# Kernel optimization log

Measured on AMD Instinct MI355X. Metric: run time of the kernel, lower is better.

The kernel has to match this reference:

```python
import jax, jax.numpy as jnp
import numpy as np

B, L, D = 8, 1024, 512
H, DK, DV = 8, 64, 64
EPS = 1e-6
NEG = -1e9


def setup_inputs() -> dict:
    key = jax.random.key(0)
    ks = jax.random.split(key, 12)
    def xavier(k, shape):
        fan_out, fan_in = shape
        bound = float(np.sqrt(6.0 / (fan_in + fan_out)))
        return jax.random.uniform(k, shape, jnp.float32, -bound, bound)
    return {
        "q": jax.random.normal(ks[0], (B, L, D), jnp.float32),
        "k": jax.random.normal(ks[1], (B, L, D), jnp.float32),
        "v": jax.random.normal(ks[2], (B, L, D), jnp.float32),
        "event_type": jax.random.randint(ks[3], (B, L), 0, 2, jnp.int32),
        "mask": jax.random.randint(ks[4], (B, L, L), 0, 2, jnp.int32).astype(bool),
        "w_qs": xavier(ks[5], (H * DK, D)),
        "w_ex_en_qs": xavier(ks[6], (H * DK, D)),
        "w_ks": xavier(ks[7], (H * DK, D)),
        "w_vs": xavier(ks[8], (H * DV, D)),
        "w_fc": xavier(ks[9], (D, H * DV)),
        "b_fc": jnp.zeros((D,), jnp.float32),
        "ln_gamma": jnp.ones((D,), jnp.float32),
        "ln_beta": jnp.zeros((D,), jnp.float32),
    }


def _layer_norm(x, gamma, beta):
    mu = jnp.mean(x, axis=-1, keepdims=True)
    var = jnp.var(x, axis=-1, keepdims=True)
    return (x - mu) * jax.lax.rsqrt(var + EPS) * gamma + beta


def reference(q, k, v, event_type, mask, w_qs, w_ex_en_qs, w_ks, w_vs, w_fc, b_fc, ln_gamma, ln_beta):
    residual = q
    qn = _layer_norm(q, ln_gamma, ln_beta)  # normalize_before=True

    # event-type flags: en_en = prev is en AND present is en; ex_en = prev is ex AND present is en
    is_en = event_type != 0                                   # [B, L]
    en_en = (is_en[:, :, None] & is_en[:, None, :])[:, None]  # [B, 1, L, L]
    ex_en = ((~is_en)[:, :, None] & is_en[:, None, :])[:, None]

    def proj(x, w, d):  # torch Linear: x @ w.T, then split heads -> [B, H, L, d]
        return (x @ w.T).reshape(B, L, H, d).transpose(0, 2, 1, 3)

    q_en = proj(qn, w_qs, DK)
    q_ex = proj(qn, w_ex_en_qs, DK)
    kh = proj(k, w_ks, DK)
    vh = proj(v, w_vs, DV)

    temp = jnp.asarray(DK ** 0.5, qn.dtype)
    scores_en = jnp.einsum('bhqd,bhkd->bhqk', q_en / temp, kh)
    scores_en = jnp.where(mask[:, None], NEG, scores_en)      # masked branch
    scores_ex = jnp.einsum('bhqd,bhkd->bhqk', q_ex / temp, kh)  # unmasked branch

    blended = en_en * scores_en + ex_en * scores_ex           # [B, H, L, L]
    attn = jax.nn.softmax(blended, axis=-1)

    out = jnp.einsum('bhqk,bhkd->bhqd', attn, vh)             # PV
    out = out.transpose(0, 2, 1, 3).reshape(B, L, H * DV)
    out = out @ w_fc.T + b_fc
    out = out + residual
    return out, attn
```

## Files before the change

### kernel.cpp

```cpp
#include <hip/hip_runtime.h>

typedef __attribute__((ext_vector_type(8))) short bf16x8;
typedef __attribute__((ext_vector_type(4))) float f32x4;

#define DEVI static __device__ __forceinline__

constexpr float NEGV = -1e9f;

DEVI unsigned short f2b(float f) {
  union { float f; unsigned int u; } c; c.f = f;
  unsigned int lsb = (c.u >> 16) & 1u;
  return (unsigned short)((c.u + 0x7fffu + lsb) >> 16);
}
DEVI float sb2f(short s) {
  union { unsigned int u; float f; } c;
  c.u = ((unsigned int)(unsigned short)s) << 16;
  return c.f;
}

DEVI void gload16(const unsigned short* g, unsigned short* l) {
  __builtin_amdgcn_global_load_lds(
      (const __attribute__((address_space(1))) unsigned int*)g,
      (__attribute__((address_space(3))) unsigned int*)l, 16, 0, 0);
}

#define KSYNC(N) asm volatile("s_waitcnt vmcnt(" #N ") lgkmcnt(0)\n\ts_barrier" ::: "memory")

__global__ void mask_detect(const unsigned int* __restrict__ m, int n, int* flag) {
  unsigned int v = 0;
  for (int i = blockIdx.x * blockDim.x + threadIdx.x; i < n; i += gridDim.x * blockDim.x)
    v |= m[i];
  if (v & ~1u) atomicOr(flag, 1);
}

__global__ void mask_canon_bits(const void* __restrict__ mraw, unsigned int* __restrict__ mb,
                                int nwords, const int* __restrict__ flag) {
  int i = blockIdx.x * blockDim.x + threadIdx.x;
  if (i >= nwords) return;
  bool isbytes = (*flag != 0);
  unsigned int out = 0;
  if (isbytes) {
    const unsigned int* p = (const unsigned int*)mraw + (size_t)i * 8;
    #pragma unroll
    for (int w = 0; w < 8; w++) {
      unsigned int bw = p[w];
      out |= ((bw & 1u) << (w * 4)) | (((bw >> 8) & 1u) << (w * 4 + 1)) |
             (((bw >> 16) & 1u) << (w * 4 + 2)) | (((bw >> 24) & 1u) << (w * 4 + 3));
    }
  } else {
    const int4* p = (const int4*)mraw + (size_t)i * 8;
    #pragma unroll
    for (int w = 0; w < 8; w++) {
      int4 v = p[w];
      out |= ((v.x != 0 ? 1u : 0u) << (w * 4)) | ((v.y != 0 ? 1u : 0u) << (w * 4 + 1)) |
             ((v.z != 0 ? 1u : 0u) << (w * 4 + 2)) | ((v.w != 0 ? 1u : 0u) << (w * 4 + 3));
    }
  }
  mb[i] = out;
}

__global__ __launch_bounds__(256) void ln_kernel(const float* __restrict__ q,
    const float* __restrict__ gamma, const float* __restrict__ beta,
    unsigned short* __restrict__ qn) {
  int row = blockIdx.x;
  int t = threadIdx.x;
  const float* x = q + (size_t)row * 512;
  float2 v = reinterpret_cast<const float2*>(x)[t];
  float s = v.x + v.y, s2 = v.x * v.x + v.y * v.y;
  #pragma unroll
  for (int o = 32; o; o >>= 1) { s += __shfl_xor(s, o); s2 += __shfl_xor(s2, o); }
  __shared__ float ls[4], ls2[4];
  int w = t >> 6;
  if ((t & 63) == 0) { ls[w] = s; ls2[w] = s2; }
  __syncthreads();
  float S = ls[0] + ls[1] + ls[2] + ls[3];
  float S2 = ls2[0] + ls2[1] + ls2[2] + ls2[3];
  float mu = S * (1.f / 512.f);
  float var = S2 * (1.f / 512.f) - mu * mu;
  float r = rsqrtf(var + 1e-6f);
  float g0 = gamma[t * 2], g1 = gamma[t * 2 + 1];
  float b0 = beta[t * 2], b1 = beta[t * 2 + 1];
  ushort2 o;
  o.x = f2b((v.x - mu) * r * g0 + b0);
  o.y = f2b((v.y - mu) * r * g1 + b1);
  reinterpret_cast<ushort2*>(qn + (size_t)row * 512)[t] = o;
}

template<int MODE, bool CVX, bool CVW>
__global__ __launch_bounds__(256) void gemm_bt(
    const void* __restrict__ Xv,
    const void* __restrict__ Wv,
    void* __restrict__ Yv,
    float scale,
    const float* __restrict__ bias,
    const float* __restrict__ resid) {
  constexpr int LDT = 40;
  __shared__ __align__(16) unsigned short lA[64 * LDT];
  __shared__ __align__(16) unsigned short lB[64 * LDT];
  int t = threadIdx.x;
  int w = t >> 6, l = t & 63, lr = l & 15, lg = l >> 4;
  int mb = blockIdx.x * 64, nb = blockIdx.y * 64;
  f32x4 acc[4];
  #pragma unroll
  for (int n = 0; n < 4; n++) acc[n] = {0.f, 0.f, 0.f, 0.f};
  int sr = t >> 2, sc = (t & 3) * 8;
  for (int k0 = 0; k0 < 512; k0 += 32) {
    __syncthreads();
    if constexpr (CVX) {
      const float* src = (const float*)Xv + (size_t)(mb + sr) * 512 + k0 + sc;
      float4 x0 = *reinterpret_cast<const float4*>(src);
      float4 x1 = *reinterpret_cast<const float4*>(src + 4);
      ushort4 h0{f2b(x0.x), f2b(x0.y), f2b(x0.z), f2b(x0.w)};
      ushort4 h1{f2b(x1.x), f2b(x1.y), f2b(x1.z), f2b(x1.w)};
      *reinterpret_cast<ushort4*>(&lA[sr * LDT + sc]) = h0;
      *reinterpret_cast<ushort4*>(&lA[sr * LDT + sc + 4]) = h1;
    } else {
      *reinterpret_cast<float4*>(&lA[sr * LDT + sc]) =
          *reinterpret_cast<const float4*>((const unsigned short*)Xv + (size_t)(mb + sr) * 512 + k0 + sc);
    }
    if constexpr (CVW) {
      const float* src = (const float*)Wv + (size_t)(nb + sr) * 512 + k0 + sc;
      float4 x0 = *reinterpret_cast<const float4*>(src);
      float4 x1 = *reinterpret_cast<const float4*>(src + 4);
      ushort4 h0{f2b(x0.x), f2b(x0.y), f2b(x0.z), f2b(x0.w)};
      ushort4 h1{f2b(x1.x), f2b(x1.y), f2b(x1.z), f2b(x1.w)};
      *reinterpret_cast<ushort4*>(&lB[sr * LDT + sc]) = h0;
      *reinterpret_cast<ushort4*>(&lB[sr * LDT + sc + 4]) = h1;
    } else {
      *reinterpret_cast<float4*>(&lB[sr * LDT + sc]) =
          *reinterpret_cast<const float4*>((const unsigned short*)Wv + (size_t)(nb + sr) * 512 + k0 + sc);
    }
    __syncthreads();
    bf16x8 a = *reinterpret_cast<const bf16x8*>(&lA[(w * 16 + lr) * LDT + lg * 8]);
    #pragma unroll
    for (int n = 0; n < 4; n++) {
      bf16x8 bb = *reinterpret_cast<const bf16x8*>(&lB[(n * 16 + lr) * LDT + lg * 8]);
      acc[n] = __builtin_amdgcn_mfma_f32_16x16x32_bf16(a, bb, acc[n], 0, 0, 0);
    }
  }
  #pragma unroll
  for (int n = 0; n < 4; n++) {
    #pragma unroll
    for (int j = 0; j < 4; j++) {
      int m = mb + w * 16 + lg * 4 + j;
      int c = nb + n * 16 + lr;
      float val = acc[n][j] * scale;
      if constexpr (MODE == 0) {
        reinterpret_cast<unsigned short*>(Yv)[(size_t)m * 512 + c] = f2b(val);
      } else if constexpr (MODE == 1) {
        int bb_ = m >> 10, ll = m & 1023, hh = c >> 6, dd = c & 63;
        reinterpret_cast<unsigned short*>(Yv)[((size_t)((bb_ * 8 + hh) * 64 + dd)) * 1024 + ll] = f2b(val);
      } else {
        reinterpret_cast<float*>(Yv)[(size_t)m * 512 + c] =
            val + bias[c] + resid[(size_t)m * 512 + c];
      }
    }
  }
}

__global__ __launch_bounds__(256) void attn_kernel(
    const unsigned short* __restrict__ qen,
    const unsigned short* __restrict__ qex,
    const unsigned short* __restrict__ kh,
    const unsigned short* __restrict__ vhT,
    const int* __restrict__ etype,
    const unsigned int* __restrict__ mbits,
    float* __restrict__ attn_g,
    unsigned short* __restrict__ pv_out) {
  int lid = blockIdx.x;
  int xcd = lid & 7, slot = lid >> 3;
  int qt = slot & 15;
  int g = ((slot >> 4) << 3) | xcd;
  int h = g & 7, b = g >> 3;

  int t = threadIdx.x, w = t >> 6, l = t & 63, lr = l & 15, lg = l >> 4;
  __shared__ unsigned int ekbits[32];
  __shared__ unsigned int mkill[64 * 33];
  __shared__ __align__(16) unsigned short klds[2][2048];
  __shared__ __align__(16) unsigned short vlds[2][2048];
  __shared__ __align__(16) unsigned short pbuf[4][16][40];

  int qb = qt * 64 + w * 16;
  int qrowA = qb + lr;
  bool evA = etype[b * 1024 + qrowA] != 0;
  const unsigned short* qp = evA ? qen : qex;
  size_t qoff = (size_t)(b * 1024 + qrowA) * 512 + h * 64;
  bf16x8 a0 = *reinterpret_cast<const bf16x8*>(qp + qoff + lg * 8);
  bf16x8 a1 = *reinterpret_cast<const bf16x8*>(qp + qoff + 32 + lg * 8);

  if (t < 32) {
    unsigned int wdd = 0;
    const int4* ep = (const int4*)(etype + b * 1024 + t * 32);
    #pragma unroll
    for (int j4 = 0; j4 < 8; j4++) {
      int4 e = ep[j4];
      wdd |= ((e.x != 0 ? 1u : 0u) << (j4 * 4)) | ((e.y != 0 ? 1u : 0u) << (j4 * 4 + 1)) |
             ((e.z != 0 ? 1u : 0u) << (j4 * 4 + 2)) | ((e.w != 0 ? 1u : 0u) << (j4 * 4 + 3));
    }
    ekbits[t] = wdd;
  }
  {
    const unsigned int* mslice = mbits + ((size_t)(b * 1024 + qt * 64)) * 32;
    for (int i = t; i < 2048; i += 256) {
      int row = i >> 5, wd = i & 31;
      bool evq_row = etype[b * 1024 + qt * 64 + row] != 0;
      mkill[row * 33 + wd] = evq_row ? mslice[i] : 0u;
    }
  }

  int qrc[4], qlc[4];
  #pragma unroll
  for (int j = 0; j < 4; j++) { qlc[j] = w * 16 + lg * 4 + j; qrc[j] = qt * 64 + qlc[j]; }

  int srow = t >> 3, sb8 = t & 7;
  const unsigned short* kgsrc = kh + ((size_t)(b * 1024) + srow) * 512 + h * 64
                                + ((sb8 ^ (srow & 7)) << 3);
  int vrow = t >> 2, vb4 = t & 3;
  const unsigned short* vb_base = vhT + ((size_t)((b * 8 + h) * 64)) * 1024;
  const unsigned short* vgsrc = vb_base + (size_t)vrow * 1024 + ((vb4 ^ ((vrow >> 1) & 3)) << 3);
  int wofs = (t & 192) * 8;

  float srun[4] = {0.f, 0.f, 0.f, 0.f};
  float rS[4];
  f32x4 oacc[4];
  #pragma unroll
  for (int n = 0; n < 4; n++) oacc[n] = {0.f, 0.f, 0.f, 0.f};
  float* ag = attn_g + ((size_t)(b * 8 + h)) * 1024 * 1024;
  float* agrow = ag + (size_t)(qb + lr) * 1024 + lg * 8;

  auto computeP1 = [&](int c) {
    int kb = c & 1;
    #pragma unroll
    for (int c2 = 0; c2 < 2; ++c2) {
      int row = c2 * 16 + lr, r7 = row & 7;
      bf16x8 b0 = *reinterpret_cast<const bf16x8*>(&klds[kb][row * 64 + ((lg ^ r7) << 3)]);
      bf16x8 b1 = *reinterpret_cast<const bf16x8*>(&klds[kb][row * 64 + (((4 + lg) ^ r7) << 3)]);
      f32x4 cc = {0.f, 0.f, 0.f, 0.f};
      cc = __builtin_amdgcn_mfma_f32_16x16x32_bf16(a0, b0, cc, 0, 0, 0);
      cc = __builtin_amdgcn_mfma_f32_16x16x32_bf16(a1, b1, cc, 0, 0, 0);
      int bitpos = (c2 << 4) + lr;
      bool ekb = (ekbits[c] >> bitpos) & 1;
      #pragma unroll
      for (int j = 0; j < 4; j++) {
        bool mk = (mkill[qlc[j] * 33 + c] >> bitpos) & 1;
        float val = ekb ? (mk ? NEGV : cc[j]) : 0.f;
        srun[j] += __expf(val);
      }
    }
  };

  auto computeP2 = [&](int c) {
    int kb = c & 1;
    #pragma unroll
    for (int c2 = 0; c2 < 2; ++c2) {
      int row = c2 * 16 + lr, r7 = row & 7;
      bf16x8 b0 = *reinterpret_cast<const bf16x8*>(&klds[kb][row * 64 + ((lg ^ r7) << 3)]);
      bf16x8 b1 = *reinterpret_cast<const bf16x8*>(&klds[kb][row * 64 + (((4 + lg) ^ r7) << 3)]);
      f32x4 cc = {0.f, 0.f, 0.f, 0.f};
      cc = __builtin_amdgcn_mfma_f32_16x16x32_bf16(a0, b0, cc, 0, 0, 0);
      cc = __builtin_amdgcn_mfma_f32_16x16x32_bf16(a1, b1, cc, 0, 0, 0);
      int bitpos = (c2 << 4) + lr;
      bool ekb = (ekbits[c] >> bitpos) & 1;
      #pragma unroll
      for (int j = 0; j < 4; j++) {
        bool mk = (mkill[qlc[j] * 33 + c] >> bitpos) & 1;
        float val = ekb ? (mk ? NEGV : cc[j]) : 0.f;
        float p = __expf(val) * rS[j];
        pbuf[w][lg * 4 + j][(c2 << 4) + lr] = f2b(p);
      }
      if (c2) {
        bf16x8 pa = *reinterpret_cast<const bf16x8*>(&pbuf[w][lr][lg * 8]);
        f32x4 f0, f1;
        f0[0] = sb2f(pa[0]); f0[1] = sb2f(pa[1]); f0[2] = sb2f(pa[2]); f0[3] = sb2f(pa[3]);
        f1[0] = sb2f(pa[4]); f1[1] = sb2f(pa[5]); f1[2] = sb2f(pa[6]); f1[3] = sb2f(pa[7]);
        __builtin_nontemporal_store(f0, reinterpret_cast<f32x4*>(agrow + c * 32));
        __builtin_nontemporal_store(f1, reinterpret_cast<f32x4*>(agrow + c * 32 + 4));
        #pragma unroll
        for (int n = 0; n < 4; n++) {
          int vr = n * 16 + lr;
          int cb = (lg ^ ((vr >> 1) & 3)) << 3;
          bf16x8 vb = *reinterpret_cast<const bf16x8*>(&vlds[kb][vr * 32 + cb]);
          oacc[n] = __builtin_amdgcn_mfma_f32_16x16x32_bf16(pa, vb, oacc[n], 0, 0, 0);
        }
      }
    }
  };

  gload16(kgsrc, &klds[0][wofs]);
  KSYNC(0);
  for (int c = 0; c < 31; ++c) {
    gload16(kgsrc + (size_t)(c + 1) * 32 * 512, &klds[(c + 1) & 1][wofs]);
    if (c > 0) { KSYNC(1); } else { asm volatile("s_waitcnt lgkmcnt(0)" ::: "memory"); }
    computeP1(c);
    __builtin_amdgcn_s_barrier();
  }
  KSYNC(0);
  computeP1(31);

  #pragma unroll
  for (int j = 0; j < 4; j++) {
    float s = srun[j];
    s += __shfl_xor(s, 1); s += __shfl_xor(s, 2);
    s += __shfl_xor(s, 4); s += __shfl_xor(s, 8);
    rS[j] = 1.f / s;
  }
  __syncthreads();

  gload16(kgsrc, &klds[0][wofs]);
  gload16(vgsrc, &vlds[0][wofs]);
  __syncthreads();

  for (int c = 0; c < 32; ++c) {
    if (c < 31) {
      gload16(kgsrc + (size_t)(c + 1) * 32 * 512, &klds[(c + 1) & 1][wofs]);
      gload16(vgsrc + (size_t)(c + 1) * 32, &vlds[(c + 1) & 1][wofs]);
    }
    computeP2(c);
    __syncthreads();
  }

  #pragma unroll
  for (int n = 0; n < 4; n++) {
    #pragma unroll
    for (int j = 0; j < 4; j++) {
      __builtin_nontemporal_store(f2b(oacc[n][j]),
          &pv_out[(size_t)(b * 1024 + qrc[j]) * 512 + h * 64 + n * 16 + lr]);
    }
  }
}

extern "C" void kernel_launch(void* const* d_in, const int* in_sizes, int n_in,
                              void* d_out, int out_size, void* d_ws, size_t ws_size,
                              hipStream_t stream) {
  (void)in_sizes; (void)n_in; (void)out_size; (void)ws_size;
  const float* q     = (const float*)d_in[0];
  const float* k     = (const float*)d_in[1];
  const float* v     = (const float*)d_in[2];
  const int* etype   = (const int*)d_in[3];
  const void* mask_raw = d_in[4];
  const float* w_qs  = (const float*)d_in[5];
  const float* w_ex  = (const float*)d_in[6];
  const float* w_ks  = (const float*)d_in[7];
  const float* w_vs  = (const float*)d_in[8];
  const float* w_fc  = (const float*)d_in[9];
  const float* b_fc  = (const float*)d_in[10];
  const float* gamma = (const float*)d_in[11];
  const float* beta  = (const float*)d_in[12];

  char* ws = (char*)d_ws;
  const size_t MB = 1024 * 1024;
  unsigned short* qn   = (unsigned short*)(ws);
  unsigned short* qen  = (unsigned short*)(ws + 8 * MB);
  unsigned short* qex  = (unsigned short*)(ws + 16 * MB);
  unsigned short* khb  = (unsigned short*)(ws + 24 * MB);
  unsigned short* vhT  = (unsigned short*)(ws + 32 * MB);
  unsigned short* ao   = (unsigned short*)(ws + 40 * MB);
  unsigned int* mbits  = (unsigned int*)(ws + 48 * MB);
  int* mflag           = (int*)(ws + 49 * MB);

  float* outp = (float*)d_out;
  float* attn_g = outp + (size_t)8 * 1024 * 512;

  ln_kernel<<<8192, 256, 0, stream>>>(q, gamma, beta, qn);

  const int MASK_N = 8 * 1024 * 1024;
  hipMemsetAsync(mflag, 0, 4, stream);
  mask_detect<<<2048, 256, 0, stream>>>((const unsigned int*)mask_raw, MASK_N / 4, mflag);
  const int NWORDS = MASK_N / 32;
  mask_canon_bits<<<(NWORDS + 255) / 256, 256, 0, stream>>>(mask_raw, mbits, NWORDS, mflag);

  dim3 gg(128, 8);
  gemm_bt<0, false, true><<<gg, 256, 0, stream>>>(qn, w_qs, qen, 0.125f, nullptr, nullptr);
  gemm_bt<0, false, true><<<gg, 256, 0, stream>>>(qn, w_ex, qex, 0.125f, nullptr, nullptr);
  gemm_bt<0, true,  true><<<gg, 256, 0, stream>>>(k,  w_ks, khb, 1.0f, nullptr, nullptr);
  gemm_bt<1, true,  true><<<gg, 256, 0, stream>>>(v,  w_vs, vhT, 1.0f, nullptr, nullptr);

  attn_kernel<<<dim3(1024), 256, 0, stream>>>(qen, qex, khb, vhT, etype, mbits,
                                              attn_g, ao);

  gemm_bt<2, false, true><<<gg, 256, 0, stream>>>(ao, w_fc, outp, 1.0f, b_fc, q);
}
```

Measured before the change: 288.4 us.

## Enlarge attention tiles to 128 queries and 64-key chunks with 512-thread blocks

The attention kernel now runs 512 threads per block (8 waves), each block covering 128 query rows, and streams K/V in 64-key chunks instead of 32, which halves the grid and the number of loop iterations and barriers. Each K/V tile loaded into LDS is reused by twice as many query rows, cutting global traffic for K/V. The custom partial waitcnt barrier is replaced with plain __syncthreads. In exchange, LDS use per block grows and the grid is smaller, so fewer blocks are resident per CU and latency hiding may drop.

```diff
diff --git a/kernel.cpp b/kernel.cpp
--- a/kernel.cpp
+++ b/kernel.cpp
@@ -23,8 +23,6 @@
       (const __attribute__((address_space(1))) unsigned int*)g,
       (__attribute__((address_space(3))) unsigned int*)l, 16, 0, 0);
 }
-
-#define KSYNC(N) asm volatile("s_waitcnt vmcnt(" #N ") lgkmcnt(0)\n\ts_barrier" ::: "memory")
 
 __global__ void mask_detect(const unsigned int* __restrict__ m, int n, int* flag) {
   unsigned int v = 0;
@@ -158,7 +156,7 @@
   }
 }
 
-__global__ __launch_bounds__(256) void attn_kernel(
+__global__ __launch_bounds__(512) void attn_kernel(
     const unsigned short* __restrict__ qen,
     const unsigned short* __restrict__ qex,
     const unsigned short* __restrict__ kh,
@@ -169,18 +167,18 @@
     unsigned short* __restrict__ pv_out) {
   int lid = blockIdx.x;
   int xcd = lid & 7, slot = lid >> 3;
-  int qt = slot & 15;
-  int g = ((slot >> 4) << 3) | xcd;
+  int qt8 = slot & 7;
+  int g = ((slot >> 3) << 3) | xcd;
   int h = g & 7, b = g >> 3;
 
   int t = threadIdx.x, w = t >> 6, l = t & 63, lr = l & 15, lg = l >> 4;
   __shared__ unsigned int ekbits[32];
-  __shared__ unsigned int mkill[64 * 33];
-  __shared__ __align__(16) unsigned short klds[2][2048];
-  __shared__ __align__(16) unsigned short vlds[2][2048];
-  __shared__ __align__(16) unsigned short pbuf[4][16][40];
-
-  int qb = qt * 64 + w * 16;
+  __shared__ unsigned int mkill[128 * 33];
+  __shared__ __align__(16) unsigned short klds[2][64 * 64];
+  __shared__ __align__(16) unsigned short vlds[2][64 * 64];
+  __shared__ __align__(16) unsigned short pbuf[8][16][40];
+
+  int qb = qt8 * 128 + w * 16;
   int qrowA = qb + lr;
   bool evA = etype[b * 1024 + qrowA] != 0;
   const unsigned short* qp = evA ? qen : qex;
@@ -200,25 +198,25 @@
     ekbits[t] = wdd;
   }
   {
-    const unsigned int* mslice = mbits + ((size_t)(b * 1024 + qt * 64)) * 32;
-    for (int i = t; i < 2048; i += 256) {
+    const unsigned int* mslice = mbits + ((size_t)(b * 1024 + qt8 * 128)) * 32;
+    for (int i = t; i < 4096; i += 512) {
       int row = i >> 5, wd = i & 31;
-      bool evq_row = etype[b * 1024 + qt * 64 + row] != 0;
+      bool evq_row = etype[b * 1024 + qt8 * 128 + row] != 0;
       mkill[row * 33 + wd] = evq_row ? mslice[i] : 0u;
     }
   }
 
   int qrc[4], qlc[4];
   #pragma unroll
-  for (int j = 0; j < 4; j++) { qlc[j] = w * 16 + lg * 4 + j; qrc[j] = qt * 64 + qlc[j]; }
+  for (int j = 0; j < 4; j++) { qlc[j] = w * 16 + lg * 4 + j; qrc[j] = qt8 * 128 + qlc[j]; }
 
   int srow = t >> 3, sb8 = t & 7;
   const unsigned short* kgsrc = kh + ((size_t)(b * 1024) + srow) * 512 + h * 64
                                 + ((sb8 ^ (srow & 7)) << 3);
-  int vrow = t >> 2, vb4 = t & 3;
+  int vrow = t >> 3, vb8 = t & 7;
   const unsigned short* vb_base = vhT + ((size_t)((b * 8 + h) * 64)) * 1024;
-  const unsigned short* vgsrc = vb_base + (size_t)vrow * 1024 + ((vb4 ^ ((vrow >> 1) & 3)) << 3);
-  int wofs = (t & 192) * 8;
+  const unsigned short* vgsrc = vb_base + (size_t)vrow * 1024 + ((vb8 ^ (vrow & 7)) << 3);
+  int wofs = (t & 448) * 8;
 
   float srun[4] = {0.f, 0.f, 0.f, 0.f};
   float rS[4];
@@ -231,18 +229,18 @@
   auto computeP1 = [&](int c) {
     int kb = c & 1;
     #pragma unroll
-    for (int c2 = 0; c2 < 2; ++c2) {
-      int row = c2 * 16 + lr, r7 = row & 7;
+    for (int kt = 0; kt < 4; ++kt) {
+      int row = kt * 16 + lr, r7 = row & 7;
       bf16x8 b0 = *reinterpret_cast<const bf16x8*>(&klds[kb][row * 64 + ((lg ^ r7) << 3)]);
       bf16x8 b1 = *reinterpret_cast<const bf16x8*>(&klds[kb][row * 64 + (((4 + lg) ^ r7) << 3)]);
       f32x4 cc = {0.f, 0.f, 0.f, 0.f};
       cc = __builtin_amdgcn_mfma_f32_16x16x32_bf16(a0, b0, cc, 0, 0, 0);
       cc = __builtin_amdgcn_mfma_f32_16x16x32_bf16(a1, b1, cc, 0, 0, 0);
-      int bitpos = (c2 << 4) + lr;
-      bool ekb = (ekbits[c] >> bitpos) & 1;
+      int wd = c * 2 + (kt >> 1), bitpos = ((kt & 1) << 4) + lr;
+      bool ekb = (ekbits[wd] >> bitpos) & 1;
       #pragma unroll
       for (int j = 0; j < 4; j++) {
-        bool mk = (mkill[qlc[j] * 33 + c] >> bitpos) & 1;
+        bool mk = (mkill[qlc[j] * 33 + wd] >> bitpos) & 1;
         float val = ekb ? (mk ? NEGV : cc[j]) : 0.f;
         srun[j] += __expf(val);
       }
@@ -252,34 +250,36 @@
   auto computeP2 = [&](int c) {
     int kb = c & 1;
     #pragma unroll
-    for (int c2 = 0; c2 < 2; ++c2) {
-      int row = c2 * 16 + lr, r7 = row & 7;
+    for (int kt = 0; kt < 4; ++kt) {
+      int row = kt * 16 + lr, r7 = row & 7;
       bf16x8 b0 = *reinterpret_cast<const bf16x8*>(&klds[kb][row * 64 + ((lg ^ r7) << 3)]);
       bf16x8 b1 = *reinterpret_cast<const bf16x8*>(&klds[kb][row * 64 + (((4 + lg) ^ r7) << 3)]);
       f32x4 cc = {0.f, 0.f, 0.f, 0.f};
       cc = __builtin_amdgcn_mfma_f32_16x16x32_bf16(a0, b0, cc, 0, 0, 0);
       cc = __builtin_amdgcn_mfma_f32_16x16x32_bf16(a1, b1, cc, 0, 0, 0);
-      int bitpos = (c2 << 4) + lr;
-      bool ekb = (ekbits[c] >> bitpos) & 1;
+      int wd = c * 2 + (kt >> 1), bitpos = ((kt & 1) << 4) + lr;
+      bool ekb = (ekbits[wd] >> bitpos) & 1;
       #pragma unroll
       for (int j = 0; j < 4; j++) {
-        bool mk = (mkill[qlc[j] * 33 + c] >> bitpos) & 1;
+        bool mk = (mkill[qlc[j] * 33 + wd] >> bitpos) & 1;
         float val = ekb ? (mk ? NEGV : cc[j]) : 0.f;
         float p = __expf(val) * rS[j];
-        pbuf[w][lg * 4 + j][(c2 << 4) + lr] = f2b(p);
+        pbuf[w][lg * 4 + j][((kt & 1) << 4) + lr] = f2b(p);
       }
-      if (c2) {
+      if (kt & 1) {
+        int ks = kt >> 1;
         bf16x8 pa = *reinterpret_cast<const bf16x8*>(&pbuf[w][lr][lg * 8]);
         f32x4 f0, f1;
         f0[0] = sb2f(pa[0]); f0[1] = sb2f(pa[1]); f0[2] = sb2f(pa[2]); f0[3] = sb2f(pa[3]);
         f1[0] = sb2f(pa[4]); f1[1] = sb2f(pa[5]); f1[2] = sb2f(pa[6]); f1[3] = sb2f(pa[7]);
-        __builtin_nontemporal_store(f0, reinterpret_cast<f32x4*>(agrow + c * 32));
-        __builtin_nontemporal_store(f1, reinterpret_cast<f32x4*>(agrow + c * 32 + 4));
+        float* dst = agrow + c * 64 + ks * 32;
+        __builtin_nontemporal_store(f0, reinterpret_cast<f32x4*>(dst));
+        __builtin_nontemporal_store(f1, reinterpret_cast<f32x4*>(dst + 4));
         #pragma unroll
         for (int n = 0; n < 4; n++) {
           int vr = n * 16 + lr;
-          int cb = (lg ^ ((vr >> 1) & 3)) << 3;
-          bf16x8 vb = *reinterpret_cast<const bf16x8*>(&vlds[kb][vr * 32 + cb]);
+          int jb = ks * 4 + lg;
+          bf16x8 vb = *reinterpret_cast<const bf16x8*>(&vlds[kb][vr * 64 + ((jb ^ (vr & 7)) << 3)]);
           oacc[n] = __builtin_amdgcn_mfma_f32_16x16x32_bf16(pa, vb, oacc[n], 0, 0, 0);
         }
       }
@@ -287,15 +287,12 @@
   };
 
   gload16(kgsrc, &klds[0][wofs]);
-  KSYNC(0);
-  for (int c = 0; c < 31; ++c) {
-    gload16(kgsrc + (size_t)(c + 1) * 32 * 512, &klds[(c + 1) & 1][wofs]);
-    if (c > 0) { KSYNC(1); } else { asm volatile("s_waitcnt lgkmcnt(0)" ::: "memory"); }
+  __syncthreads();
+  for (int c = 0; c < 16; ++c) {
+    if (c < 15) gload16(kgsrc + (size_t)(c + 1) * 64 * 512, &klds[(c + 1) & 1][wofs]);
     computeP1(c);
-    __builtin_amdgcn_s_barrier();
-  }
-  KSYNC(0);
-  computeP1(31);
+    __syncthreads();
+  }
 
   #pragma unroll
   for (int j = 0; j < 4; j++) {
@@ -304,16 +301,15 @@
     s += __shfl_xor(s, 4); s += __shfl_xor(s, 8);
     rS[j] = 1.f / s;
   }
-  __syncthreads();
 
   gload16(kgsrc, &klds[0][wofs]);
   gload16(vgsrc, &vlds[0][wofs]);
   __syncthreads();
 
-  for (int c = 0; c < 32; ++c) {
-    if (c < 31) {
-      gload16(kgsrc + (size_t)(c + 1) * 32 * 512, &klds[(c + 1) & 1][wofs]);
-      gload16(vgsrc + (size_t)(c + 1) * 32, &vlds[(c + 1) & 1][wofs]);
+  for (int c = 0; c < 16; ++c) {
+    if (c < 15) {
+      gload16(kgsrc + (size_t)(c + 1) * 64 * 512, &klds[(c + 1) & 1][wofs]);
+      gload16(vgsrc + (size_t)(c + 1) * 64, &vlds[(c + 1) & 1][wofs]);
     }
     computeP2(c);
     __syncthreads();
@@ -375,8 +371,8 @@
   gemm_bt<0, true,  true><<<gg, 256, 0, stream>>>(k,  w_ks, khb, 1.0f, nullptr, nullptr);
   gemm_bt<1, true,  true><<<gg, 256, 0, stream>>>(v,  w_vs, vhT, 1.0f, nullptr, nullptr);
 
-  attn_kernel<<<dim3(1024), 256, 0, stream>>>(qen, qex, khb, vhT, etype, mbits,
-                                              attn_g, ao);
+  attn_kernel<<<dim3(512), 512, 0, stream>>>(qen, qex, khb, vhT, etype, mbits,
+                                             attn_g, ao);
 
   gemm_bt<2, false, true><<<gg, 256, 0, stream>>>(ao, w_fc, outp, 1.0f, b_fc, q);
 }
```

Measured after the change: 316.9 us. 1.1x slower.
